# Optimization experiments

Measured on AMD Instinct MI355X. Metric: run time of the kernel, lower is better.

## Reference

```python
import jax, jax.numpy as jnp
import numpy as np


def _lsap_np(cost):
    """Jonker-Volgenant / Hungarian (e-maxx formulation) for a square cost
    matrix. Returns col_of_row: row i is assigned to column col_of_row[i].
    Matches scipy.optimize.linear_sum_assignment on square matrices."""
    cost = np.asarray(cost, dtype=np.float64)
    n = cost.shape[0]
    u = np.zeros(n + 1)
    v = np.zeros(n + 1)
    p = np.zeros(n + 1, dtype=np.int64)   # p[j] = row assigned to column j (1-based; 0 = none)
    way = np.zeros(n + 1, dtype=np.int64)
    for i in range(1, n + 1):
        p[0] = i
        j0 = 0
        minv = np.full(n + 1, np.inf)
        used = np.zeros(n + 1, dtype=bool)
        while True:
            used[j0] = True
            i0 = p[j0]
            js = np.nonzero(~used[1:])[0] + 1  # unused columns (vectorized inner loop)
            cur = cost[i0 - 1, js - 1] - u[i0] - v[js]
            better = cur < minv[js]
            minv[js] = np.where(better, cur, minv[js])
            way[js] = np.where(better, j0, way[js])
            j1 = js[np.argmin(minv[js])]
            delta = minv[j1]
            u[p[used]] += delta          # rows assigned to used columns are distinct
            v[used] -= delta
            minv[~used] -= delta
            j0 = j1
            if p[j0] == 0:
                break
        # augment along the alternating path
        while j0 != 0:
            j1 = way[j0]
            p[j0] = p[j1]
            j0 = j1
    col_of_row = np.zeros(n, dtype=np.int32)
    for j in range(1, n + 1):
        if p[j] > 0:
            col_of_row[p[j] - 1] = j - 1
    return col_of_row


def _batched_lsap_host(dists):
    dists = np.asarray(dists)
    return np.stack([_lsap_np(d) for d in dists]).astype(np.int32)  # [B, N]


def _pairwise_dist(y_true, y_pred):
    # dist[b, i, j] = || y_true[b, i] - y_pred[b, j] ||_2, matching tf.norm(..., axis=-1)
    diff = y_true[:, :, None, :] - y_pred[:, None, :, :]  # [B, N, N, D]
    return jnp.sqrt(jnp.sum(diff * diff, axis=-1))        # [B, N, N]


def setup_inputs() -> dict:
    key = jax.random.key(0)
    k1, k2 = jax.random.split(key)
    B, N, D = 64, 128, 64
    y_true = jax.random.normal(k1, (B, N, D), dtype=jnp.float32)
    y_pred = jax.random.normal(k2, (B, N, D), dtype=jnp.float32)
    return {"y_true": y_true, "y_pred": y_pred}


def reference(y_true, y_pred):
    dist = _pairwise_dist(y_true, y_pred)                      # [B, N, N]
    B, N = dist.shape[0], dist.shape[1]
    col_ind = jax.pure_callback(
        _batched_lsap_host,
        jax.ShapeDtypeStruct((B, N), jnp.int32),
        jax.lax.stop_gradient(dist),
    )                                                          # [B, N]
    matched = jnp.take_along_axis(dist, col_ind[:, :, None].astype(jnp.int32), axis=2)[..., 0]
    batch_losses = jnp.sum(matched, axis=1)                    # [B]
    return jnp.mean(batch_losses)
```

## Files before the change

### kernel.cpp

```cpp
#include <hip/hip_runtime.h>
#include <math.h>
#include <stdint.h>

#define BATCH 64
#define N 128
#define DIM 64
#define ARR_CAP 640

typedef unsigned uint32x2_t __attribute__((ext_vector_type(2)));

__device__ __forceinline__ unsigned monokey(float x) {
    unsigned b = __float_as_uint(x);
    return b ^ (unsigned)(((int)b >> 31) | (int)0x80000000u);
}

__device__ __forceinline__ unsigned umin_(unsigned a, unsigned b) { return a < b ? a : b; }
__device__ __forceinline__ unsigned umax_(unsigned a, unsigned b) { return a > b ? a : b; }
__device__ __forceinline__ int rfl(int v) { return __builtin_amdgcn_readfirstlane(v); }
__device__ __forceinline__ int rl_i(int v, int l) { return __builtin_amdgcn_readlane(v, l); }
__device__ __forceinline__ float rl_f(float v, int l) {
    return __int_as_float(__builtin_amdgcn_readlane(__float_as_int(v), l));
}

#define DPP_ROR(x, n) __builtin_amdgcn_update_dpp((int)(x), (int)(x), 0x120 + (n), 0xF, 0xF, false)

__device__ __forceinline__ unsigned wave_kmin(unsigned k) {
    unsigned a = (unsigned)DPP_ROR(k, 1);
    unsigned b = (unsigned)DPP_ROR(k, 2);
    k = umin_(k, umin_(a, b));
    a = (unsigned)DPP_ROR(k, 3);
    b = (unsigned)DPP_ROR(k, 6);
    k = umin_(k, umin_(a, b));
    a = (unsigned)DPP_ROR(k, 9);
    k = umin_(k, a);
#if __has_builtin(__builtin_amdgcn_permlane16_swap)
    { uint32x2_t r = __builtin_amdgcn_permlane16_swap(k, k, false, false); k = umin_(r[0], r[1]); }
#else
    k = umin_(k, (unsigned)__shfl_xor((int)k, 16));
#endif
#if __has_builtin(__builtin_amdgcn_permlane32_swap)
    { uint32x2_t r = __builtin_amdgcn_permlane32_swap(k, k, false, false); k = umin_(r[0], r[1]); }
#else
    k = umin_(k, (unsigned)__shfl_xor((int)k, 32));
#endif
    return k;
}

__device__ __forceinline__ void wave_kmin2(unsigned& ks, unsigned& kb, int lane) {
    unsigned ps, pb;
#define KM2_COMBINE { unsigned ns = umin_(ks, ps); kb = umin_(umin_(kb, pb), umax_(ks, ps)); ks = ns; }
    ps = (unsigned)DPP_ROR(ks, 1); pb = (unsigned)DPP_ROR(kb, 1); KM2_COMBINE;
    ps = (unsigned)DPP_ROR(ks, 2); pb = (unsigned)DPP_ROR(kb, 2); KM2_COMBINE;
    ps = (unsigned)DPP_ROR(ks, 4); pb = (unsigned)DPP_ROR(kb, 4); KM2_COMBINE;
    ps = (unsigned)DPP_ROR(ks, 8); pb = (unsigned)DPP_ROR(kb, 8); KM2_COMBINE;
#if __has_builtin(__builtin_amdgcn_permlane16_swap)
    {
        uint32x2_t rs = __builtin_amdgcn_permlane16_swap(ks, ks, false, false);
        uint32x2_t rb = __builtin_amdgcn_permlane16_swap(kb, kb, false, false);
        ps = (lane & 16) ? rs[0] : rs[1]; pb = (lane & 16) ? rb[0] : rb[1];
    }
    KM2_COMBINE;
#else
    ps = (unsigned)__shfl_xor((int)ks, 16); pb = (unsigned)__shfl_xor((int)kb, 16); KM2_COMBINE;
#endif
#if __has_builtin(__builtin_amdgcn_permlane32_swap)
    {
        uint32x2_t rs = __builtin_amdgcn_permlane32_swap(ks, ks, false, false);
        uint32x2_t rb = __builtin_amdgcn_permlane32_swap(kb, kb, false, false);
        ps = (lane & 32) ? rs[0] : rs[1]; pb = (lane & 32) ? rb[0] : rb[1];
    }
    KM2_COMBINE;
#else
    ps = (unsigned)__shfl_xor((int)ks, 32); pb = (unsigned)__shfl_xor((int)kb, 32); KM2_COMBINE;
#endif
#undef KM2_COMBINE
}

__global__ __launch_bounds__(64, 1)
void lsap_kernel(const float* __restrict__ y_true, const float* __restrict__ y_pred,
                 float* __restrict__ batch_sums, float* __restrict__ out, int use_atomic) {
    __shared__ float dist[N * N];
    __shared__ float ytl[N * DIM];
    __shared__ int unlist[N + ARR_CAP + 8];

    const int b = blockIdx.x;
    const int lane = threadIdx.x;
    const int ca = lane, cb = lane + 64;
    const int ja = lane + 1, jb = lane + 65;

    {
        const float4* yt4 = (const float4*)(y_true + (size_t)b * N * DIM);
        float4* ytl4 = (float4*)ytl;
        for (int k = lane; k < N * DIM / 4; k += 64) ytl4[k] = yt4[k];
    }

    float ypa[DIM], ypb[DIM];
    {
        const float4* pa4 = (const float4*)(y_pred + (size_t)b * N * DIM + (size_t)ca * DIM);
        const float4* pb4 = (const float4*)(y_pred + (size_t)b * N * DIM + (size_t)cb * DIM);
        #pragma unroll
        for (int k = 0; k < DIM / 4; ++k) {
            float4 v4 = pa4[k];
            ypa[4*k+0]=v4.x; ypa[4*k+1]=v4.y; ypa[4*k+2]=v4.z; ypa[4*k+3]=v4.w;
            float4 w4 = pb4[k];
            ypb[4*k+0]=w4.x; ypb[4*k+1]=w4.y; ypb[4*k+2]=w4.z; ypb[4*k+3]=w4.w;
        }
    }
    __syncthreads();

    float va = INFINITY, vb = INFINITY;
    for (int i = 0; i < N; ++i) {
        const float4* yr = (const float4*)(ytl + i * DIM);
        float a0 = 0.f, a1 = 0.f;
        #pragma unroll
        for (int k = 0; k < DIM / 4; ++k) {
            float4 t4 = yr[k];
            float d;
            d = t4.x - ypa[4*k+0]; a0 = fmaf(d, d, a0);
            d = t4.y - ypa[4*k+1]; a0 = fmaf(d, d, a0);
            d = t4.z - ypa[4*k+2]; a0 = fmaf(d, d, a0);
            d = t4.w - ypa[4*k+3]; a0 = fmaf(d, d, a0);
            d = t4.x - ypb[4*k+0]; a1 = fmaf(d, d, a1);
            d = t4.y - ypb[4*k+1]; a1 = fmaf(d, d, a1);
            d = t4.z - ypb[4*k+2]; a1 = fmaf(d, d, a1);
            d = t4.w - ypb[4*k+3]; a1 = fmaf(d, d, a1);
        }
        float d0 = sqrtf(a0), d1 = sqrtf(a1);
        dist[i * N + ca] = d0;
        dist[i * N + cb] = d1;
        va = fminf(va, d0);
        vb = fminf(vb, d1);
    }

    int   pa = 0, pb = 0;
    float upa = 0.f, upb = 0.f;
    float ura = 0.f, urb = 0.f;
    int   waya = 0, wayb = 0;

    int nun = 0;
    float pd0 = dist[ca], pd1 = dist[cb];
    for (int r = 0; r < N; ++r) {
        float c0 = pd0 - va, c1 = pd1 - vb;
        if (r + 1 < N) { pd0 = dist[(r+1) * N + ca]; pd1 = dist[(r+1) * N + cb]; }
        unsigned k0 = (monokey(c0) & ~0x7Fu) | (unsigned)lane;
        unsigned k1 = (monokey(c1) & ~0x7Fu) | 64u | (unsigned)lane;
        unsigned ks = umin_(k0, k1), kb2 = umax_(k0, k1);
        wave_kmin2(ks, kb2, lane);
        int s1 = rfl((int)ks);
        int s2 = rfl((int)kb2);
        int w1 = s1 & 63, cb1 = (s1 >> 6) & 1;
        float u1 = rl_f(cb1 ? c1 : c0, w1);
        float u2 = rl_f(((s2 >> 6) & 1) ? c1 : c0, s2 & 63);
        int j1 = 1 + w1 + (cb1 << 6);
        int pj1 = rl_i(cb1 ? pb : pa, w1);
        if (pj1 == 0) {
            float dd = u2 - u1;
            if (ja == j1) { pa = r + 1; upa = u2; va -= dd; }
            if (jb == j1) { pb = r + 1; upb = u2; vb -= dd; }
            if ((r & 63) == lane) { if (r < 64) ura = u2; else urb = u2; }
        } else {
            unlist[nun] = r;
            ++nun;
            if ((r & 63) == lane) { if (r < 64) ura = u1; else urb = u1; }
        }
    }

    int qk = 0, nf = nun;
    {
        int ops = 0;
        int icur = -1;
        float d0c = 0.f, d1c = 0.f;
        int qi = -1; float qd0 = 0.f, qd1 = 0.f;
        if (nun > 0) {
            icur = rfl(unlist[0]); qk = 1;
            d0c = dist[icur * N + ca]; d1c = dist[icur * N + cb];
            if (qk < nf) { qi = rfl(unlist[qk]); qd0 = dist[qi * N + ca]; qd1 = dist[qi * N + cb]; }
        }
        while (icur >= 0 && ops < ARR_CAP) {
            ++ops;
            float c0 = d0c - va, c1 = d1c - vb;
            unsigned k0 = (monokey(c0) & ~0x7Fu) | (unsigned)lane;
            unsigned k1 = (monokey(c1) & ~0x7Fu) | 64u | (unsigned)lane;
            unsigned ks = umin_(k0, k1), kb2 = umax_(k0, k1);
            wave_kmin2(ks, kb2, lane);
            int s1 = rfl((int)ks);
            int s2 = rfl((int)kb2);
            int w1 = s1 & 63, cb1 = (s1 >> 6) & 1;
            int w2 = s2 & 63, cb2 = (s2 >> 6) & 1;
            int pj1 = rl_i(cb1 ? pb : pa, w1);
            int pj2 = rl_i(cb2 ? pb : pa, w2);
            float sa0 = 0.f, sa1 = 0.f, sb0 = 0.f, sb1 = 0.f;
            if (pj1) { sa0 = dist[(pj1 - 1) * N + ca]; sa1 = dist[(pj1 - 1) * N + cb]; }
            if (pj2) { sb0 = dist[(pj2 - 1) * N + ca]; sb1 = dist[(pj2 - 1) * N + cb]; }
            float u1 = rl_f(cb1 ? c1 : c0, w1);
            float u2 = rl_f(cb2 ? c1 : c0, w2);
            int j1 = 1 + w1 + (cb1 << 6);
            int j2 = 1 + w2 + (cb2 << 6);
            bool transfer = (u1 < u2);
            int jt, it0;
            if (transfer) {
                float dd = u2 - u1;
                if (ja == j1) va -= dd;
                if (jb == j1) vb -= dd;
                jt = j1; it0 = pj1;
            } else if (pj1 > 0) { jt = j2; it0 = pj2; }
            else { jt = j1; it0 = 0; }

            if (ja == jt) { pa = icur + 1; upa = u2; }
            if (jb == jt) { pb = icur + 1; upb = u2; }
            if ((icur & 63) == lane) { if (icur < 64) ura = u2; else urb = u2; }

            if (transfer && it0 > 0) {
                icur = it0 - 1; d0c = sa0; d1c = sa1;
            } else {
                if (!transfer && pj1 > 0) { unlist[nf] = it0 - 1; ++nf; }
                if (qk < nf) {
                    if (qi < 0) { icur = it0 - 1; d0c = sb0; d1c = sb1; }
                    else        { icur = qi;      d0c = qd0; d1c = qd1; }
                    ++qk;
                    if (qk < nf) {
                        qi = rfl(unlist[qk]);
                        qd0 = dist[qi * N + ca]; qd1 = dist[qi * N + cb];
                    } else qi = -1;
                } else icur = -1;
            }
        }
        if (icur >= 0) { --qk; unlist[qk] = icur; }
    }

    for (int t = qk; t < nf; ++t) {
        int r = rfl(unlist[t]);
        float d0 = dist[r * N + ca], d1 = dist[r * N + cb];
        float u_i = rl_f((r >= 64) ? urb : ura, r & 63);
        float mina = INFINITY, minb = INFINITY;
        int useda = 0, usedb = 0;
        waya = 0; wayb = 0;
        float uacca = 0.f, uaccb = 0.f;
        float u_acc_i = u_i;
        float u0c = u_i;
        int j0 = 0;

        for (int it = 0; it < 2 * N; ++it) {
            if (ja == j0) useda = 1;
            if (jb == j0) usedb = 1;
            if (!useda) { float cur = d0 - u0c - va; if (cur < mina) { mina = cur; waya = j0; } }
            if (!usedb) { float cur = d1 - u0c - vb; if (cur < minb) { minb = cur; wayb = j0; } }

            float fa_ = useda ? INFINITY : mina;
            float fb_ = usedb ? INFINITY : minb;
            unsigned kA = (monokey(fa_) & 0xFFFF8000u) | ((unsigned)pa << 7) | (unsigned)lane;
            unsigned kB = (monokey(fb_) & 0xFFFF8000u) | ((unsigned)pb << 7) | 64u | (unsigned)lane;
            unsigned kk = wave_kmin(umin_(kA, kB));
            int s = rfl((int)kk);
            int i1 = (s >> 7) & 0xFF;

            float nd0 = 0.f, nd1 = 0.f;
            if (i1) { nd0 = dist[(i1 - 1) * N + ca]; nd1 = dist[(i1 - 1) * N + cb]; }

            int w = s & 63, cbw = (s >> 6) & 1;
            float delta = rl_f(cbw ? fb_ : fa_, w);
            float u1v = rl_f(cbw ? upb : upa, w);

            if (useda) { va -= delta; uacca += delta; } else { mina -= delta; }
            if (usedb) { vb -= delta; uaccb += delta; } else { minb -= delta; }
            u_acc_i += delta;

            j0 = 1 + w + (cbw << 6);
            if (i1 == 0) break;
            u0c = u1v; d0 = nd0; d1 = nd1;
        }

        if (useda) upa += uacca;
        if (usedb) upb += uaccb;

        int jj = j0;
        for (int hop = 0; hop < N + 1; ++hop) {
            int wj = (jj - 1) & 63;
            int sbj = (jj > 64) ? 1 : 0;
            int jp = rl_i(sbj ? wayb : waya, wj);
            int np; float nu;
            if (jp == 0) { np = r + 1; nu = u_acc_i; }
            else {
                int wp = (jp - 1) & 63;
                int sbp = (jp > 64) ? 1 : 0;
                np = rl_i(sbp ? pb : pa, wp);
                nu = rl_f(sbp ? upb : upa, wp);
            }
            if (ja == jj) { pa = np; upa = nu; }
            if (jb == jj) { pb = np; upb = nu; }
            if (jp == 0) break;
            jj = jp;
        }
    }

    float s = dist[(pa - 1) * N + ca] + dist[(pb - 1) * N + cb];
    #pragma unroll
    for (int m = 1; m < 64; m <<= 1) s += __shfl_xor(s, m);
    if (lane == 0) {
        if (use_atomic) atomicAdd(out, s * (1.0f / (float)BATCH));
        else batch_sums[b] = s;
    }
}

__global__ __launch_bounds__(64)
void reduce_kernel(const float* __restrict__ bs, float* __restrict__ out) {
    int tid = threadIdx.x;
    float v = bs[tid];
    #pragma unroll
    for (int m = 1; m < 64; m <<= 1) v += __shfl_xor(v, m);
    if (tid == 0) out[0] = v * (1.0f / (float)BATCH);
}

extern "C" void kernel_launch(void* const* d_in, const int* in_sizes, int n_in,
                              void* d_out, int out_size, void* d_ws, size_t ws_size,
                              hipStream_t stream) {
    const float* y_true = (const float*)d_in[0];
    const float* y_pred = (const float*)d_in[1];
    float* out = (float*)d_out;

    if (ws_size >= BATCH * sizeof(float)) {
        float* bs = (float*)d_ws;
        lsap_kernel<<<BATCH, 64, 0, stream>>>(y_true, y_pred, bs, out, 0);
        reduce_kernel<<<1, 64, 0, stream>>>(bs, out);
    } else {
        hipMemsetAsync(d_out, 0, sizeof(float), stream);
        lsap_kernel<<<BATCH, 64, 0, stream>>>(y_true, y_pred, nullptr, out, 1);
    }
}
```

Baseline: 592.4 us.

## Warm-start Hungarian with auction rounds to precompute column prices

Adds a bounded auction phase (up to a fixed number of rounds with two epsilon levels) before the Hungarian solve. Free rows bid on their best columns via LDS atomics, which sets column prices and a near-complete assignment. A reduced-cost pass then initialises row potentials and a greedy matching, replacing the per-row wave-min column reduction. The goal is fewer augmenting-path iterations in the serial JV loop. The cost is extra O(N^2) sweeps per round, and optimality of the result depends on the potentials remaining dual-feasible for the later augmentation.

```diff
diff --git a/kernel.cpp b/kernel.cpp
--- a/kernel.cpp
+++ b/kernel.cpp
@@ -6,12 +6,17 @@
 #define N 128
 #define DIM 64
 #define ARR_CAP 640
+#define AUCTION_ROUNDS 26
 
 typedef unsigned uint32x2_t __attribute__((ext_vector_type(2)));
 
 __device__ __forceinline__ unsigned monokey(float x) {
     unsigned b = __float_as_uint(x);
     return b ^ (unsigned)(((int)b >> 31) | (int)0x80000000u);
+}
+__device__ __forceinline__ float monoval(unsigned k) {
+    unsigned b = (k & 0x80000000u) ? (k & 0x7FFFFFFFu) : ~k;
+    return __uint_as_float(b);
 }
 
 __device__ __forceinline__ unsigned umin_(unsigned a, unsigned b) { return a < b ? a : b; }
@@ -81,6 +86,9 @@
                  float* __restrict__ batch_sums, float* __restrict__ out, int use_atomic) {
     __shared__ float dist[N * N];
     __shared__ float ytl[N * DIM];
+    __shared__ float v_lds[N];
+    __shared__ unsigned bid[N];
+    __shared__ int rowfree[N];
     __shared__ int unlist[N + ARR_CAP + 8];
 
     const int b = blockIdx.x;
@@ -132,36 +140,103 @@
         vb = fminf(vb, d1);
     }
 
+    {
+        int ow_a = -1, ow_b = -1;
+        rowfree[lane] = 1; rowfree[lane + 64] = 1;
+        for (int rd = 0; rd < AUCTION_ROUNDS; ++rd) {
+            float eps = (rd < 8) ? 0.5f : 0.08f;
+            v_lds[ca] = va; v_lds[cb] = vb;
+            bid[ca] = 0xFFFFFFFFu; bid[cb] = 0xFFFFFFFFu;
+            __syncthreads();
+            int f0 = rowfree[lane], f1 = rowfree[lane + 64];
+            int f = __popcll(__ballot(f0)) + __popcll(__ballot(f1));
+            if (f <= 4) break;
+            if (f0) {
+                const float* dr = dist + lane * N;
+                float m1 = INFINITY, m2 = INFINITY; int j1 = 0;
+                #pragma unroll 4
+                for (int t = 0; t < N; ++t) {
+                    int j = (t + lane) & (N - 1);
+                    float c = dr[j] - v_lds[j];
+                    float mx = fmaxf(m1, c);
+                    m2 = fminf(m2, mx);
+                    if (c < m1) { m1 = c; j1 = j; }
+                }
+                float newv = v_lds[j1] - (m2 - m1) - eps;
+                atomicMin(&bid[j1], (monokey(newv) & ~127u) | (unsigned)lane);
+            }
+            if (f1) {
+                const float* dr = dist + (lane + 64) * N;
+                float m1 = INFINITY, m2 = INFINITY; int j1 = 0;
+                #pragma unroll 4
+                for (int t = 0; t < N; ++t) {
+                    int j = (t + lane) & (N - 1);
+                    float c = dr[j] - v_lds[j];
+                    float mx = fmaxf(m1, c);
+                    m2 = fminf(m2, mx);
+                    if (c < m1) { m1 = c; j1 = j; }
+                }
+                float newv = v_lds[j1] - (m2 - m1) - eps;
+                atomicMin(&bid[j1], (monokey(newv) & ~127u) | (unsigned)(lane + 64));
+            }
+            __syncthreads();
+            unsigned w0 = bid[ca];
+            if (w0 != 0xFFFFFFFFu) {
+                int wr = (int)(w0 & 127u);
+                if (ow_a >= 0) rowfree[ow_a] = 1;
+                rowfree[wr] = 0;
+                ow_a = wr;
+                va = monoval(w0 & ~127u);
+            }
+            unsigned w1 = bid[cb];
+            if (w1 != 0xFFFFFFFFu) {
+                int wr = (int)(w1 & 127u);
+                if (ow_b >= 0) rowfree[ow_b] = 1;
+                rowfree[wr] = 0;
+                ow_b = wr;
+                vb = monoval(w1 & ~127u);
+            }
+        }
+    }
+
+    v_lds[ca] = va; v_lds[cb] = vb;
+    __syncthreads();
+    float m1a = INFINITY, m1b = INFINITY;
+    int j1a = 0, j1b = 0;
+    {
+        const float* dra = dist + lane * N;
+        const float* drb = dist + (lane + 64) * N;
+        #pragma unroll 4
+        for (int t = 0; t < N; ++t) {
+            int j = (t + lane) & (N - 1);
+            float vj = v_lds[j];
+            float c0 = dra[j] - vj;
+            float c1 = drb[j] - vj;
+            if (c0 < m1a) { m1a = c0; j1a = j; }
+            if (c1 < m1b) { m1b = c1; j1b = j; }
+        }
+    }
+    float ura = m1a, urb = m1b;
+
     int   pa = 0, pb = 0;
     float upa = 0.f, upb = 0.f;
-    float ura = 0.f, urb = 0.f;
     int   waya = 0, wayb = 0;
 
     int nun = 0;
-    float pd0 = dist[ca], pd1 = dist[cb];
     for (int r = 0; r < N; ++r) {
-        float c0 = pd0 - va, c1 = pd1 - vb;
-        if (r + 1 < N) { pd0 = dist[(r+1) * N + ca]; pd1 = dist[(r+1) * N + cb]; }
-        unsigned k0 = (monokey(c0) & ~0x7Fu) | (unsigned)lane;
-        unsigned k1 = (monokey(c1) & ~0x7Fu) | 64u | (unsigned)lane;
-        unsigned ks = umin_(k0, k1), kb2 = umax_(k0, k1);
-        wave_kmin2(ks, kb2, lane);
-        int s1 = rfl((int)ks);
-        int s2 = rfl((int)kb2);
-        int w1 = s1 & 63, cb1 = (s1 >> 6) & 1;
-        float u1 = rl_f(cb1 ? c1 : c0, w1);
-        float u2 = rl_f(((s2 >> 6) & 1) ? c1 : c0, s2 & 63);
-        int j1 = 1 + w1 + (cb1 << 6);
-        int pj1 = rl_i(cb1 ? pb : pa, w1);
-        if (pj1 == 0) {
-            float dd = u2 - u1;
-            if (ja == j1) { pa = r + 1; upa = u2; va -= dd; }
-            if (jb == j1) { pb = r + 1; upb = u2; vb -= dd; }
-            if ((r & 63) == lane) { if (r < 64) ura = u2; else urb = u2; }
+        int w = r & 63, hi = r >> 6;
+        int j1 = rl_i(hi ? j1b : j1a, w);
+        float u1 = rl_f(hi ? m1b : m1a, w);
+        int cw = j1 & 63, cs = j1 >> 6;
+        int pj = rl_i(cs ? pb : pa, cw);
+        if (pj == 0) {
+            if (lane == cw) {
+                if (cs) { pb = r + 1; upb = u1; }
+                else    { pa = r + 1; upa = u1; }
+            }
         } else {
             unlist[nun] = r;
             ++nun;
-            if ((r & 63) == lane) { if (r < 64) ura = u1; else urb = u1; }
         }
     }
 
```

After: 692.7 us. 1.17x slower.

## Replace per-row augmentation with multi-source shortest augmenting path phases

Applied to the files above, without the earlier changes.

After the greedy and auction-style phases, the remaining unassigned rows are no longer augmented one at a time. Each phase seeds a Dijkstra-like search from all free rows at once, with the initial minima taken over every free row and the source row recorded as a negative way index. Augmentation stops at whichever free row the path reaches, and the duals of all free rows are shifted by the accumulated delta. This aims to shorten individual searches, but each phase pays a seeding scan over all free rows, and the tie-breaking may differ from the sequential reference.

```diff
diff --git a/kernel.cpp b/kernel.cpp
--- a/kernel.cpp
+++ b/kernel.cpp
@@ -82,6 +82,7 @@
     __shared__ float dist[N * N];
     __shared__ float ytl[N * DIM];
     __shared__ int unlist[N + ARR_CAP + 8];
+    __shared__ int flags[N];
 
     const int b = blockIdx.x;
     const int lane = threadIdx.x;
@@ -135,7 +136,6 @@
     int   pa = 0, pb = 0;
     float upa = 0.f, upb = 0.f;
     float ura = 0.f, urb = 0.f;
-    int   waya = 0, wayb = 0;
 
     int nun = 0;
     float pd0 = dist[ca], pd1 = dist[cb];
@@ -165,9 +165,8 @@
         }
     }
 
-    int qk = 0, nf = nun;
-    {
-        int ops = 0;
+    {
+        int qk = 0, nf = nun, ops = 0;
         int icur = -1;
         float d0c = 0.f, d1c = 0.f;
         int qi = -1; float qd0 = 0.f, qd1 = 0.f;
@@ -225,27 +224,49 @@
                 } else icur = -1;
             }
         }
-        if (icur >= 0) { --qk; unlist[qk] = icur; }
-    }
-
-    for (int t = qk; t < nf; ++t) {
-        int r = rfl(unlist[t]);
-        float d0 = dist[r * N + ca], d1 = dist[r * N + cb];
-        float u_i = rl_f((r >= 64) ? urb : ura, r & 63);
+    }
+
+    flags[lane] = 0; flags[lane + 64] = 0;
+    __syncthreads();
+    if (pa) flags[pa - 1] = 1;
+    if (pb) flags[pb - 1] = 1;
+    __syncthreads();
+    int fra = flags[lane] ^ 1;
+    int frb = flags[lane + 64] ^ 1;
+
+    for (int phase = 0; phase < N; ++phase) {
+        unsigned long long m0 = __ballot(fra), m1 = __ballot(frb);
+        if (!(m0 | m1)) break;
+
         float mina = INFINITY, minb = INFINITY;
+        int waya = 0, wayb = 0;
+        unsigned long long mm = m0;
+        while (mm) {
+            int r = (int)(__ffsll(mm) - 1); mm &= mm - 1;
+            float ur = rl_f(ura, r);
+            float q0 = dist[r * N + ca] - ur;
+            float q1 = dist[r * N + cb] - ur;
+            if (q0 < mina) { mina = q0; waya = -(r + 1); }
+            if (q1 < minb) { minb = q1; wayb = -(r + 1); }
+        }
+        mm = m1;
+        while (mm) {
+            int rr = (int)(__ffsll(mm) - 1); mm &= mm - 1;
+            float ur = rl_f(urb, rr);
+            int r = rr + 64;
+            float q0 = dist[r * N + ca] - ur;
+            float q1 = dist[r * N + cb] - ur;
+            if (q0 < mina) { mina = q0; waya = -(r + 1); }
+            if (q1 < minb) { minb = q1; wayb = -(r + 1); }
+        }
+        mina -= va; minb -= vb;
+
         int useda = 0, usedb = 0;
-        waya = 0; wayb = 0;
         float uacca = 0.f, uaccb = 0.f;
-        float u_acc_i = u_i;
-        float u0c = u_i;
+        float dsum = 0.f;
         int j0 = 0;
 
         for (int it = 0; it < 2 * N; ++it) {
-            if (ja == j0) useda = 1;
-            if (jb == j0) usedb = 1;
-            if (!useda) { float cur = d0 - u0c - va; if (cur < mina) { mina = cur; waya = j0; } }
-            if (!usedb) { float cur = d1 - u0c - vb; if (cur < minb) { minb = cur; wayb = j0; } }
-
             float fa_ = useda ? INFINITY : mina;
             float fb_ = usedb ? INFINITY : minb;
             unsigned kA = (monokey(fa_) & 0xFFFF8000u) | ((unsigned)pa << 7) | (unsigned)lane;
@@ -253,34 +274,42 @@
             unsigned kk = wave_kmin(umin_(kA, kB));
             int s = rfl((int)kk);
             int i1 = (s >> 7) & 0xFF;
-
-            float nd0 = 0.f, nd1 = 0.f;
-            if (i1) { nd0 = dist[(i1 - 1) * N + ca]; nd1 = dist[(i1 - 1) * N + cb]; }
-
             int w = s & 63, cbw = (s >> 6) & 1;
+            int jn = 1 + w + (cbw << 6);
+            int ipf = (i1 ? i1 : 1) - 1;
+            float d0 = dist[ipf * N + ca], d1 = dist[ipf * N + cb];
             float delta = rl_f(cbw ? fb_ : fa_, w);
-            float u1v = rl_f(cbw ? upb : upa, w);
+            float u0c = rl_f(cbw ? upb : upa, w);
 
             if (useda) { va -= delta; uacca += delta; } else { mina -= delta; }
             if (usedb) { vb -= delta; uaccb += delta; } else { minb -= delta; }
-            u_acc_i += delta;
-
-            j0 = 1 + w + (cbw << 6);
+            dsum += delta;
+            if (ja == jn) useda = 1;
+            if (jb == jn) usedb = 1;
+            j0 = jn;
             if (i1 == 0) break;
-            u0c = u1v; d0 = nd0; d1 = nd1;
+
+            if (!useda) { float cur = d0 - u0c - va; if (cur < mina) { mina = cur; waya = jn; } }
+            if (!usedb) { float cur = d1 - u0c - vb; if (cur < minb) { minb = cur; wayb = jn; } }
         }
 
         if (useda) upa += uacca;
         if (usedb) upb += uaccb;
+        if (fra) ura += dsum;
+        if (frb) urb += dsum;
 
         int jj = j0;
-        for (int hop = 0; hop < N + 1; ++hop) {
+        for (int hop = 0; hop <= N; ++hop) {
             int wj = (jj - 1) & 63;
             int sbj = (jj > 64) ? 1 : 0;
             int jp = rl_i(sbj ? wayb : waya, wj);
             int np; float nu;
-            if (jp == 0) { np = r + 1; nu = u_acc_i; }
-            else {
+            if (jp < 0) {
+                int rs = -jp - 1;
+                np = rs + 1;
+                nu = rl_f((rs >= 64) ? urb : ura, rs & 63);
+                if ((rs & 63) == lane) { if (rs < 64) fra = 0; else frb = 0; }
+            } else {
                 int wp = (jp - 1) & 63;
                 int sbp = (jp > 64) ? 1 : 0;
                 np = rl_i(sbp ? pb : pa, wp);
@@ -288,7 +317,7 @@
             }
             if (ja == jj) { pa = np; upa = nu; }
             if (jb == jj) { pb = np; upb = nu; }
-            if (jp == 0) break;
+            if (jp < 0) break;
             jj = jp;
         }
     }
```

Result: slower. 647.0 us (+9.2%).

## Use lazy dual updates in the Dijkstra phase of the augmenting search

Applied to the files above, without the earlier changes.

Rewrites the shortest-augmenting-path inner loop to track a cumulative distance instead of subtracting delta from every column's minv and v each iteration. Used columns are marked by setting minv to infinity, and dual potentials are fixed up once after the search from the recorded settle distances. The next row's dist load is issued unconditionally so the loop has fewer branches and less per-iteration arithmetic. The cost is more reliance on float reassociation, which can shift tie-breaking slightly compared with the incremental updates.

```diff
diff --git a/kernel.cpp b/kernel.cpp
--- a/kernel.cpp
+++ b/kernel.cpp
@@ -135,7 +135,6 @@
     int   pa = 0, pb = 0;
     float upa = 0.f, upb = 0.f;
     float ura = 0.f, urb = 0.f;
-    int   waya = 0, wayb = 0;
 
     int nun = 0;
     float pd0 = dist[ca], pd1 = dist[cb];
@@ -230,48 +229,55 @@
 
     for (int t = qk; t < nf; ++t) {
         int r = rfl(unlist[t]);
-        float d0 = dist[r * N + ca], d1 = dist[r * N + cb];
+        float d0s = dist[r * N + ca], d1s = dist[r * N + cb];
         float u_i = rl_f((r >= 64) ? urb : ura, r & 63);
-        float mina = INFINITY, minb = INFINITY;
-        int useda = 0, usedb = 0;
-        waya = 0; wayb = 0;
-        float uacca = 0.f, uaccb = 0.f;
-        float u_acc_i = u_i;
-        float u0c = u_i;
+
+        const float va0 = va, vb0 = vb;
+        float mina = d0s - u_i - va;
+        float minb = d1s - u_i - vb;
+        int waya = 0, wayb = 0;
+        float dsa = -1.0f, dsb = -1.0f;
+        const unsigned pka = ((unsigned)pa << 7) | (unsigned)lane;
+        const unsigned pkb = ((unsigned)pb << 7) | 64u | (unsigned)lane;
+        float dsum = 0.f;
         int j0 = 0;
 
         for (int it = 0; it < 2 * N; ++it) {
-            if (ja == j0) useda = 1;
-            if (jb == j0) usedb = 1;
-            if (!useda) { float cur = d0 - u0c - va; if (cur < mina) { mina = cur; waya = j0; } }
-            if (!usedb) { float cur = d1 - u0c - vb; if (cur < minb) { minb = cur; wayb = j0; } }
-
-            float fa_ = useda ? INFINITY : mina;
-            float fb_ = usedb ? INFINITY : minb;
-            unsigned kA = (monokey(fa_) & 0xFFFF8000u) | ((unsigned)pa << 7) | (unsigned)lane;
-            unsigned kB = (monokey(fb_) & 0xFFFF8000u) | ((unsigned)pb << 7) | 64u | (unsigned)lane;
+            unsigned kA = (monokey(mina) & 0xFFFF8000u) | pka;
+            unsigned kB = (monokey(minb) & 0xFFFF8000u) | pkb;
             unsigned kk = wave_kmin(umin_(kA, kB));
             int s = rfl((int)kk);
             int i1 = (s >> 7) & 0xFF;
-
-            float nd0 = 0.f, nd1 = 0.f;
-            if (i1) { nd0 = dist[(i1 - 1) * N + ca]; nd1 = dist[(i1 - 1) * N + cb]; }
-
             int w = s & 63, cbw = (s >> 6) & 1;
-            float delta = rl_f(cbw ? fb_ : fa_, w);
-            float u1v = rl_f(cbw ? upb : upa, w);
-
-            if (useda) { va -= delta; uacca += delta; } else { mina -= delta; }
-            if (usedb) { vb -= delta; uaccb += delta; } else { minb -= delta; }
-            u_acc_i += delta;
-
-            j0 = 1 + w + (cbw << 6);
+
+            int ip = (i1 ? i1 - 1 : 0) * N;
+            float nd0 = dist[ip + ca], nd1 = dist[ip + cb];
+
+            float mch = cbw ? minb : mina;
+            float uch = cbw ? upb : upa;
+            float ds_new = rl_f(mch, w);
+            float u0 = rl_f(uch, w);
+
+            int jn = 1 + w + (cbw << 6);
+            if (ja == jn) { mina = INFINITY; va = -INFINITY; dsa = ds_new; }
+            if (jb == jn) { minb = INFINITY; vb = -INFINITY; dsb = ds_new; }
+            dsum = ds_new;
+            j0 = jn;
             if (i1 == 0) break;
-            u0c = u1v; d0 = nd0; d1 = nd1;
-        }
-
-        if (useda) upa += uacca;
-        if (usedb) upb += uaccb;
+
+            float tt = dsum - u0;
+            float c0 = nd0 + tt - va;
+            float c1 = nd1 + tt - vb;
+            if (c0 < mina) { mina = c0; waya = jn; }
+            if (c1 < minb) { minb = c1; wayb = jn; }
+        }
+
+        float u_acc_i = u_i + dsum;
+        bool sa = (dsa >= 0.f), sb = (dsb >= 0.f);
+        va = sa ? (va0 - (dsum - dsa)) : va0;
+        vb = sb ? (vb0 - (dsum - dsb)) : vb0;
+        if (sa) upa += (dsum - dsa);
+        if (sb) upb += (dsum - dsb);
 
         int jj = j0;
         for (int hop = 0; hop < N + 1; ++hop) {
```

After: 593.0 us. Within noise of the previous version (+0.1%).
